# Optimization experiments

Hardware: AMD Instinct MI355X
Metric: run time of the kernel (lower is better)

## Reference

```python
import jax, jax.numpy as jnp
import numpy as np

N_NODES = 50000
N_EDGES = 1_600_000
IN_CH = 128
HIDDEN = 64
OUT_CH = 1


def glorot(key, shape):
    limit = np.sqrt(6.0 / (shape[0] + shape[1]))
    return jax.random.uniform(key, shape, jnp.float32, -limit, limit)


def setup_inputs() -> dict:
    key = jax.random.key(0)
    ks = jax.random.split(key, 6)
    x = jax.random.normal(ks[0], (N_NODES, IN_CH), jnp.float32)
    edge_index = jax.random.randint(ks[1], (2, N_EDGES), 0, N_NODES, jnp.int64)
    W1 = glorot(ks[2], (IN_CH, HIDDEN))
    b1 = jnp.zeros((HIDDEN,), jnp.float32)
    W2 = glorot(ks[3], (HIDDEN, HIDDEN // 2))
    b2 = jnp.zeros((HIDDEN // 2,), jnp.float32)
    Wh = glorot(ks[4], (HIDDEN // 2, OUT_CH))
    bh = jnp.zeros((OUT_CH,), jnp.float32)
    return {"x": x, "edge_index": edge_index, "W1": W1, "b1": b1,
            "W2": W2, "b2": b2, "Wh": Wh, "bh": bh}


def gcn_conv(x, src, dst, W, b):
    """PyG-style GCNConv: H' = D^{-1/2} (A + I) D^{-1/2} X W + b."""
    n = x.shape[0]
    h = x @ W  # transform first (smaller message dim)
    # degree of A + I (all edge weights = 1, self-loop weight = 1)
    deg = jax.ops.segment_sum(jnp.ones(src.shape[0], h.dtype), dst,
                              num_segments=n) + 1.0
    dinv = deg ** -0.5
    norm = dinv[src] * dinv[dst]                      # [E]
    msg = h[src] * norm[:, None]                      # [E, F] gather
    agg = jax.ops.segment_sum(msg, dst, num_segments=n)  # scatter-add
    agg = agg + h * (dinv * dinv)[:, None]            # self-loop term
    return agg + b


def reference(x, edge_index, W1, b1, W2, b2, Wh, bh):
    src, dst = edge_index[0], edge_index[1]
    h = jax.nn.relu(gcn_conv(x, src, dst, W1, b1))
    # dropout: inference mode (training=False) -> identity
    h = jax.nn.relu(gcn_conv(h, src, dst, W2, b2))
    return h @ Wh + bh
```

## Files before the change

### kernel.cpp

```cpp
#include <hip/hip_runtime.h>

#define N_NODES 50000
#define IN_CH 128
#define HID 64
#define HID2 32

constexpr int NB = 391;
constexpr int CHUNK = 4096;
constexpr int CAP = 5120;
#define FPSCALE 524288.0f
#define FPINV   0x1p-19f

__device__ __forceinline__ unsigned short f2bf(float f) {
    union { float f; unsigned u; } v; v.f = f;
    unsigned r = v.u + 0x7fff + ((v.u >> 16) & 1);
    return (unsigned short)(r >> 16);
}
__device__ __forceinline__ float bflo(unsigned d) {
    union { unsigned u; float f; } v; v.u = d << 16; return v.f;
}
__device__ __forceinline__ float bfhi(unsigned d) {
    union { unsigned u; float f; } v; v.u = d & 0xffff0000u; return v.f;
}

__global__ __launch_bounds__(256) void bin_kernel(const int* __restrict__ src,
                                                  const int* __restrict__ dst,
                                                  int* __restrict__ bcur,
                                                  unsigned short* __restrict__ psrc,
                                                  unsigned char* __restrict__ pbyte, int E) {
    __shared__ int hist[NB], lbase[NB], gbase[NB], lcur[NB];
    __shared__ unsigned short outs[CHUNK];
    __shared__ int outd[CHUNK];
    int tid = threadIdx.x;
    int base = blockIdx.x * CHUNK;
    int cnt = min(CHUNK, E - base);
    for (int i = tid; i < NB; i += 256) hist[i] = 0;
    int es[CHUNK / 256], ed[CHUNK / 256];
    __syncthreads();
#pragma unroll
    for (int k = 0; k < CHUNK / 256; k++) {
        int e = base + k * 256 + tid;
        if (e < E) {
            es[k] = src[e];
            ed[k] = dst[e];
            atomicAdd(&hist[ed[k] >> 7], 1);
        }
    }
    __syncthreads();
    if (tid == 0) {
        int run = 0;
        for (int b = 0; b < NB; b++) { int t = hist[b]; lbase[b] = run; run += t; }
    }
    __syncthreads();
    for (int i = tid; i < NB; i += 256) {
        gbase[i] = i * CAP + (hist[i] ? atomicAdd(&bcur[i], hist[i]) : 0);
        lcur[i] = lbase[i];
    }
    __syncthreads();
#pragma unroll
    for (int k = 0; k < CHUNK / 256; k++) {
        int e = base + k * 256 + tid;
        if (e < E) {
            int b = ed[k] >> 7;
            int p = atomicAdd(&lcur[b], 1);
            outs[p] = (unsigned short)es[k];
            outd[p] = ed[k];
        }
    }
    __syncthreads();
#pragma unroll
    for (int k = 0; k < CHUNK / 256; k++) {
        int i = k * 256 + tid;
        if (i < cnt) {
            int d = outd[i];
            int b = d >> 7;
            int gp = gbase[b] + (i - lbase[b]);
            psrc[gp] = outs[i];
            pbyte[gp] = (unsigned char)(d & 127);
        }
    }
}

__global__ __launch_bounds__(256) void fine_kernel(unsigned short* __restrict__ psrc,
                                                   const unsigned char* __restrict__ pbyte,
                                                   const int* __restrict__ bcur,
                                                   int* __restrict__ off,
                                                   unsigned short* __restrict__ len,
                                                   float* __restrict__ dinv, int N) {
    __shared__ unsigned short lsrc[CAP];
    __shared__ unsigned char lb[CAP];
    __shared__ int fh[128], fb[128], fc[128];
    int b = blockIdx.x, tid = threadIdx.x;
    int gb = b * CAP;
    int cnt = min(bcur[b], CAP);
    if (tid < 128) fh[tid] = 0;
    __syncthreads();
    for (int i = tid; i < cnt; i += 256) {
        lsrc[i] = psrc[gb + i];
        int dl = pbyte[gb + i];
        lb[i] = (unsigned char)dl;
        atomicAdd(&fh[dl], 1);
    }
    __syncthreads();
    if (tid == 0) {
        int run = 0;
        for (int j = 0; j < 128; j++) { int t = fh[j]; fb[j] = run; run += t; }
    }
    __syncthreads();
    if (tid < 128) {
        fc[tid] = fb[tid];
        int node = (b << 7) + tid;
        if (node < N) {
            off[node] = gb + fb[tid];
            len[node] = (unsigned short)fh[tid];
            dinv[node] = rsqrtf((float)fh[tid] + 1.0f);
        }
    }
    __syncthreads();
    for (int i = tid; i < cnt; i += 256) {
        int p = atomicAdd(&fc[lb[i]], 1);
        psrc[gb + p] = lsrc[i];
    }
}

template <int K, int J, int NPB>
__global__ __launch_bounds__(256) void gemm_t_kernel(const float* __restrict__ X,
                                                     const float* __restrict__ W,
                                                     const float* __restrict__ dinv,
                                                     unsigned short* __restrict__ out, int N) {
    constexpr int QJ = J / 4, GR = 256 / QJ, NPT = NPB / GR, S = NPB + 4, KC = 64;
    static_assert(NPT == 4, "float4 x-read assumes NPT==4");
    static_assert(K % KC == 0, "");
    __shared__ float Ws[K * J];
    __shared__ float Xs[KC * S];
    int tid = threadIdx.x;
    for (int i = tid; i < K * J / 4; i += 256) ((float4*)Ws)[i] = ((const float4*)W)[i];
    int n0 = blockIdx.x * NPB;
    int q = tid % QJ, g = (tid / QJ) * NPT;
    float4 acc[NPT];
#pragma unroll
    for (int t = 0; t < NPT; t++) acc[t] = make_float4(0.f, 0.f, 0.f, 0.f);
    for (int h = 0; h < K; h += KC) {
        __syncthreads();
        for (int i = tid; i < NPB * KC; i += 256) {
            int kl = i & (KC - 1), r = i >> 6;
            int n = n0 + r;
            Xs[kl * S + r] = (n < N) ? X[(size_t)n * K + h + kl] : 0.f;
        }
        __syncthreads();
#pragma unroll 8
        for (int kl = 0; kl < KC; kl++) {
            float4 w  = *(const float4*)&Ws[(h + kl) * J + q * 4];
            float4 xv = *(const float4*)&Xs[kl * S + g];
            acc[0].x += xv.x * w.x; acc[0].y += xv.x * w.y; acc[0].z += xv.x * w.z; acc[0].w += xv.x * w.w;
            acc[1].x += xv.y * w.x; acc[1].y += xv.y * w.y; acc[1].z += xv.y * w.z; acc[1].w += xv.y * w.w;
            acc[2].x += xv.z * w.x; acc[2].y += xv.z * w.y; acc[2].z += xv.z * w.z; acc[2].w += xv.z * w.w;
            acc[3].x += xv.w * w.x; acc[3].y += xv.w * w.y; acc[3].z += xv.w * w.z; acc[3].w += xv.w * w.w;
        }
    }
#pragma unroll
    for (int t = 0; t < NPT; t++) {
        int n = n0 + g + t;
        if (n < N) {
            float d0 = dinv[n] * FPSCALE;
            ushort4 o = make_ushort4(f2bf(acc[t].x * d0), f2bf(acc[t].y * d0),
                                     f2bf(acc[t].z * d0), f2bf(acc[t].w * d0));
            *(ushort4*)(out + (size_t)n * J + q * 4) = o;
        }
    }
}

__global__ __launch_bounds__(256) void agg1_kernel(const unsigned short* __restrict__ sorted_src,
                                                   const int* __restrict__ off,
                                                   const unsigned short* __restrict__ len,
                                                   const float* __restrict__ dinv,
                                                   const unsigned short* __restrict__ xws,
                                                   const float* __restrict__ b1,
                                                   float* __restrict__ h1, int N) {
    int lane = threadIdx.x & 63;
    int n = blockIdx.x * 4 + (threadIdx.x >> 6);
    if (n >= N) return;
    int g = lane >> 3, fl = lane & 7;
    int start = off[n], end = start + len[n];
    int acc[8] = {0, 0, 0, 0, 0, 0, 0, 0};
    int i = start + g;
    for (; i + 8 < end; i += 16) {
        int s0 = sorted_src[i], s1 = sorted_src[i + 8];
        uint4 q0 = *(const uint4*)(xws + (size_t)s0 * HID + fl * 8);
        uint4 q1 = *(const uint4*)(xws + (size_t)s1 * HID + fl * 8);
        acc[0] += (int)bflo(q0.x) + (int)bflo(q1.x);
        acc[1] += (int)bfhi(q0.x) + (int)bfhi(q1.x);
        acc[2] += (int)bflo(q0.y) + (int)bflo(q1.y);
        acc[3] += (int)bfhi(q0.y) + (int)bfhi(q1.y);
        acc[4] += (int)bflo(q0.z) + (int)bflo(q1.z);
        acc[5] += (int)bfhi(q0.z) + (int)bfhi(q1.z);
        acc[6] += (int)bflo(q0.w) + (int)bflo(q1.w);
        acc[7] += (int)bfhi(q0.w) + (int)bfhi(q1.w);
    }
    if (i < end) {
        int s = sorted_src[i];
        uint4 q = *(const uint4*)(xws + (size_t)s * HID + fl * 8);
        acc[0] += (int)bflo(q.x); acc[1] += (int)bfhi(q.x);
        acc[2] += (int)bflo(q.y); acc[3] += (int)bfhi(q.y);
        acc[4] += (int)bflo(q.z); acc[5] += (int)bfhi(q.z);
        acc[6] += (int)bflo(q.w); acc[7] += (int)bfhi(q.w);
    }
#pragma unroll
    for (int m = 8; m <= 32; m <<= 1)
#pragma unroll
        for (int j = 0; j < 8; j++) acc[j] += __shfl_xor(acc[j], m, 64);
    if (g == 0) {
        float dis = dinv[n] * FPINV;
        uint4 q = *(const uint4*)(xws + (size_t)n * HID + fl * 8);
        int sv[8] = {(int)bflo(q.x), (int)bfhi(q.x), (int)bflo(q.y), (int)bfhi(q.y),
                     (int)bflo(q.z), (int)bfhi(q.z), (int)bflo(q.w), (int)bfhi(q.w)};
        float4 bb0 = *(const float4*)(b1 + fl * 8);
        float4 bb1 = *(const float4*)(b1 + fl * 8 + 4);
        float bbv[8] = {bb0.x, bb0.y, bb0.z, bb0.w, bb1.x, bb1.y, bb1.z, bb1.w};
        float o[8];
#pragma unroll
        for (int j = 0; j < 8; j++)
            o[j] = fmaxf((float)(acc[j] + sv[j]) * dis + bbv[j], 0.f);
        *(float4*)(h1 + (size_t)n * HID + fl * 8)     = make_float4(o[0], o[1], o[2], o[3]);
        *(float4*)(h1 + (size_t)n * HID + fl * 8 + 4) = make_float4(o[4], o[5], o[6], o[7]);
    }
}

__global__ __launch_bounds__(256) void agg2_final_kernel(const unsigned short* __restrict__ sorted_src,
                                                         const int* __restrict__ off,
                                                         const unsigned short* __restrict__ len,
                                                         const float* __restrict__ dinv,
                                                         const unsigned short* __restrict__ hws,
                                                         const float* __restrict__ b2,
                                                         const float* __restrict__ Wh,
                                                         const float* __restrict__ bh,
                                                         float* __restrict__ out, int N) {
    int lane = threadIdx.x & 63;
    int n = blockIdx.x * 4 + (threadIdx.x >> 6);
    if (n >= N) return;
    int g = lane >> 2, fl = lane & 3;
    int start = off[n], end = start + len[n];
    int acc[8] = {0, 0, 0, 0, 0, 0, 0, 0};
    int i = start + g;
    for (; i + 16 < end; i += 32) {
        int s0 = sorted_src[i], s1 = sorted_src[i + 16];
        uint4 q0 = *(const uint4*)(hws + (size_t)s0 * HID2 + fl * 8);
        uint4 q1 = *(const uint4*)(hws + (size_t)s1 * HID2 + fl * 8);
        acc[0] += (int)bflo(q0.x) + (int)bflo(q1.x);
        acc[1] += (int)bfhi(q0.x) + (int)bfhi(q1.x);
        acc[2] += (int)bflo(q0.y) + (int)bflo(q1.y);
        acc[3] += (int)bfhi(q0.y) + (int)bfhi(q1.y);
        acc[4] += (int)bflo(q0.z) + (int)bflo(q1.z);
        acc[5] += (int)bfhi(q0.z) + (int)bfhi(q1.z);
        acc[6] += (int)bflo(q0.w) + (int)bflo(q1.w);
        acc[7] += (int)bfhi(q0.w) + (int)bfhi(q1.w);
    }
    if (i < end) {
        int s = sorted_src[i];
        uint4 q = *(const uint4*)(hws + (size_t)s * HID2 + fl * 8);
        acc[0] += (int)bflo(q.x); acc[1] += (int)bfhi(q.x);
        acc[2] += (int)bflo(q.y); acc[3] += (int)bfhi(q.y);
        acc[4] += (int)bflo(q.z); acc[5] += (int)bfhi(q.z);
        acc[6] += (int)bflo(q.w); acc[7] += (int)bfhi(q.w);
    }
#pragma unroll
    for (int m = 4; m <= 32; m <<= 1)
#pragma unroll
        for (int j = 0; j < 8; j++) acc[j] += __shfl_xor(acc[j], m, 64);
    float dis = dinv[n] * FPINV;
    uint4 q = *(const uint4*)(hws + (size_t)n * HID2 + fl * 8);
    int sv[8] = {(int)bflo(q.x), (int)bfhi(q.x), (int)bflo(q.y), (int)bfhi(q.y),
                 (int)bflo(q.z), (int)bfhi(q.z), (int)bflo(q.w), (int)bfhi(q.w)};
    float4 bb0 = *(const float4*)(b2 + fl * 8);
    float4 bb1 = *(const float4*)(b2 + fl * 8 + 4);
    float bbv[8] = {bb0.x, bb0.y, bb0.z, bb0.w, bb1.x, bb1.y, bb1.z, bb1.w};
    float4 wv0 = *(const float4*)(Wh + fl * 8);
    float4 wv1 = *(const float4*)(Wh + fl * 8 + 4);
    float wvv[8] = {wv0.x, wv0.y, wv0.z, wv0.w, wv1.x, wv1.y, wv1.z, wv1.w};
    float p = 0.f;
#pragma unroll
    for (int j = 0; j < 8; j++)
        p += fmaxf((float)(acc[j] + sv[j]) * dis + bbv[j], 0.f) * wvv[j];
    p += __shfl_xor(p, 1, 64);
    p += __shfl_xor(p, 2, 64);
    if (lane == 0) out[n] = p + bh[0];
}

extern "C" void kernel_launch(void* const* d_in, const int* in_sizes, int n_in,
                              void* d_out, int out_size, void* d_ws, size_t ws_size,
                              hipStream_t stream) {
    const float* x  = (const float*)d_in[0];
    const int*   ei = (const int*)d_in[1];
    const float* W1 = (const float*)d_in[2];
    const float* b1 = (const float*)d_in[3];
    const float* W2 = (const float*)d_in[4];
    const float* b2 = (const float*)d_in[5];
    const float* Wh = (const float*)d_in[6];
    const float* bh = (const float*)d_in[7];
    float* out = (float*)d_out;

    const int N = N_NODES;
    const int E = in_sizes[1] / 2;
    const int* src = ei;
    const int* dst = ei + E;

    int* ws = (int*)d_ws;
    int*            bcur  = ws;
    int*            off   = bcur + 512;
    unsigned short* len   = (unsigned short*)(off + 50048);
    float*          dinv  = (float*)((int*)len + 25024);
    unsigned short* psrc  = (unsigned short*)(dinv + 50048);
    unsigned char*  pbyte = (unsigned char*)(psrc + (size_t)NB * CAP);
    unsigned short* xws   = (unsigned short*)(pbyte + (size_t)NB * CAP);
    float*          h1    = (float*)(xws + (size_t)N * HID);
    unsigned short* hws   = xws;

    hipMemsetAsync(bcur, 0, NB * sizeof(int), stream);

    int eblocks = (E + CHUNK - 1) / CHUNK;
    bin_kernel<<<eblocks, 256, 0, stream>>>(src, dst, bcur, psrc, pbyte, E);
    fine_kernel<<<NB, 256, 0, stream>>>(psrc, pbyte, bcur, off, len, dinv, N);

    gemm_t_kernel<IN_CH, HID, 64><<<(N + 63) / 64, 256, 0, stream>>>(x, W1, dinv, xws, N);
    agg1_kernel<<<(N + 3) / 4, 256, 0, stream>>>(psrc, off, len, dinv, xws, b1, h1, N);

    gemm_t_kernel<HID, HID2, 128><<<(N + 127) / 128, 256, 0, stream>>>(h1, W2, dinv, hws, N);
    agg2_final_kernel<<<(N + 3) / 4, 256, 0, stream>>>(psrc, off, len, dinv, hws, b2, Wh, bh, out, N);
}
```

Measured before the change: 231.3 us.

## Rewrite dense transform GEMM with row-major XOR-swizzled shared tile and smaller blocks

Replaces the transposed shared-memory X tile (scalar global loads, transposed stores) with a row-major tile loaded by coalesced float4 reads and XOR-swizzled to avoid bank conflicts. Each thread now computes 2 nodes instead of 4, and blocks cover half as many nodes, giving more blocks and one sync instead of per-chunk syncs. The cost is less register reuse of W per thread and scalar swizzled LDS reads for X.

Result: faster. 211.8 us (-8.4%).

```diff
diff --git a/kernel.cpp b/kernel.cpp
--- a/kernel.cpp
+++ b/kernel.cpp
@@ -124,49 +124,54 @@
 }
 
 template <int K, int J, int NPB>
-__global__ __launch_bounds__(256) void gemm_t_kernel(const float* __restrict__ X,
+__global__ __launch_bounds__(256) void gemm_s_kernel(const float* __restrict__ X,
                                                      const float* __restrict__ W,
                                                      const float* __restrict__ dinv,
                                                      unsigned short* __restrict__ out, int N) {
-    constexpr int QJ = J / 4, GR = 256 / QJ, NPT = NPB / GR, S = NPB + 4, KC = 64;
-    static_assert(NPT == 4, "float4 x-read assumes NPT==4");
-    static_assert(K % KC == 0, "");
+    constexpr int QJ = J / 4;
+    constexpr int NPT = NPB / (256 / QJ);
+    static_assert(NPT == 2, "layout assumes 2 nodes/thread");
+    constexpr int RG = K / 4;
+    constexpr int RS = K + 4;
     __shared__ float Ws[K * J];
-    __shared__ float Xs[KC * S];
+    __shared__ float Xs[NPB * RS];
     int tid = threadIdx.x;
     for (int i = tid; i < K * J / 4; i += 256) ((float4*)Ws)[i] = ((const float4*)W)[i];
     int n0 = blockIdx.x * NPB;
+    for (int i = tid; i < NPB * RG; i += 256) {
+        int r = i / RG, c = i % RG;
+        int n = n0 + r;
+        float4 v = make_float4(0.f, 0.f, 0.f, 0.f);
+        if (n < N) v = ((const float4*)(X + (size_t)n * K))[c];
+        *(float4*)&Xs[r * RS + ((c ^ (r & 7)) << 2)] = v;
+    }
+    __syncthreads();
     int q = tid % QJ, g = (tid / QJ) * NPT;
-    float4 acc[NPT];
-#pragma unroll
-    for (int t = 0; t < NPT; t++) acc[t] = make_float4(0.f, 0.f, 0.f, 0.f);
-    for (int h = 0; h < K; h += KC) {
-        __syncthreads();
-        for (int i = tid; i < NPB * KC; i += 256) {
-            int kl = i & (KC - 1), r = i >> 6;
-            int n = n0 + r;
-            Xs[kl * S + r] = (n < N) ? X[(size_t)n * K + h + kl] : 0.f;
-        }
-        __syncthreads();
+    const float* xr0 = &Xs[g * RS];
+    const float* xr1 = &Xs[(g + 1) * RS];
+    int sw0 = g & 7, sw1 = (g + 1) & 7;
+    float4 a0 = make_float4(0.f, 0.f, 0.f, 0.f);
+    float4 a1 = make_float4(0.f, 0.f, 0.f, 0.f);
 #pragma unroll 8
-        for (int kl = 0; kl < KC; kl++) {
-            float4 w  = *(const float4*)&Ws[(h + kl) * J + q * 4];
-            float4 xv = *(const float4*)&Xs[kl * S + g];
-            acc[0].x += xv.x * w.x; acc[0].y += xv.x * w.y; acc[0].z += xv.x * w.z; acc[0].w += xv.x * w.w;
-            acc[1].x += xv.y * w.x; acc[1].y += xv.y * w.y; acc[1].z += xv.y * w.z; acc[1].w += xv.y * w.w;
-            acc[2].x += xv.z * w.x; acc[2].y += xv.z * w.y; acc[2].z += xv.z * w.z; acc[2].w += xv.z * w.w;
-            acc[3].x += xv.w * w.x; acc[3].y += xv.w * w.y; acc[3].z += xv.w * w.z; acc[3].w += xv.w * w.w;
-        }
-    }
-#pragma unroll
-    for (int t = 0; t < NPT; t++) {
-        int n = n0 + g + t;
-        if (n < N) {
-            float d0 = dinv[n] * FPSCALE;
-            ushort4 o = make_ushort4(f2bf(acc[t].x * d0), f2bf(acc[t].y * d0),
-                                     f2bf(acc[t].z * d0), f2bf(acc[t].w * d0));
-            *(ushort4*)(out + (size_t)n * J + q * 4) = o;
-        }
+    for (int k = 0; k < K; k++) {
+        float4 w = *(const float4*)&Ws[k * J + q * 4];
+        float x0 = xr0[(((k >> 2) ^ sw0) << 2) + (k & 3)];
+        float x1 = xr1[(((k >> 2) ^ sw1) << 2) + (k & 3)];
+        a0.x += x0 * w.x; a0.y += x0 * w.y; a0.z += x0 * w.z; a0.w += x0 * w.w;
+        a1.x += x1 * w.x; a1.y += x1 * w.y; a1.z += x1 * w.z; a1.w += x1 * w.w;
+    }
+    int n = n0 + g;
+    if (n < N) {
+        float d0 = dinv[n] * FPSCALE;
+        ushort4 o = make_ushort4(f2bf(a0.x * d0), f2bf(a0.y * d0),
+                                 f2bf(a0.z * d0), f2bf(a0.w * d0));
+        *(ushort4*)(out + (size_t)n * J + q * 4) = o;
+    }
+    if (n + 1 < N) {
+        float d1 = dinv[n + 1] * FPSCALE;
+        ushort4 o = make_ushort4(f2bf(a1.x * d1), f2bf(a1.y * d1),
+                                 f2bf(a1.z * d1), f2bf(a1.w * d1));
+        *(ushort4*)(out + (size_t)(n + 1) * J + q * 4) = o;
     }
 }
 
@@ -321,9 +326,9 @@
     bin_kernel<<<eblocks, 256, 0, stream>>>(src, dst, bcur, psrc, pbyte, E);
     fine_kernel<<<NB, 256, 0, stream>>>(psrc, pbyte, bcur, off, len, dinv, N);
 
-    gemm_t_kernel<IN_CH, HID, 64><<<(N + 63) / 64, 256, 0, stream>>>(x, W1, dinv, xws, N);
+    gemm_s_kernel<IN_CH, HID, 32><<<(N + 31) / 32, 256, 0, stream>>>(x, W1, dinv, xws, N);
     agg1_kernel<<<(N + 3) / 4, 256, 0, stream>>>(psrc, off, len, dinv, xws, b1, h1, N);
 
-    gemm_t_kernel<HID, HID2, 128><<<(N + 127) / 128, 256, 0, stream>>>(h1, W2, dinv, hws, N);
+    gemm_s_kernel<HID, HID2, 64><<<(N + 63) / 64, 256, 0, stream>>>(h1, W2, dinv, hws, N);
     agg2_final_kernel<<<(N + 3) / 4, 256, 0, stream>>>(psrc, off, len, dinv, hws, b2, Wh, bh, out, N);
 }
```
